# Performance work log

Hardware: AMD Instinct MI355X
Metric: run time of the kernel (lower is better)

The kernel has to match this reference:

```python
import jax, jax.numpy as jnp
import numpy as np
import math

B, LQ, LK = 4, 1024, 2048
QD, KD, VD = 768, 512, 512
H, NH = 1024, 16
HD = H // NH

def setup_inputs() -> dict:
    key = jax.random.key(0)
    ks = jax.random.split(key, 11)
    s = 0.02
    return {
        "query": jax.random.normal(ks[0], (B, LQ, QD), jnp.float32),
        "key": jax.random.normal(ks[1], (B, LK, KD), jnp.float32),
        "value": jax.random.normal(ks[2], (B, LK, VD), jnp.float32),
        "Wq": jax.random.normal(ks[3], (QD, H), jnp.float32) * s,
        "bq": jnp.zeros((H,), jnp.float32),
        "Wk": jax.random.normal(ks[4], (KD, H), jnp.float32) * s,
        "bk": jnp.zeros((H,), jnp.float32),
        "Wv": jax.random.normal(ks[5], (VD, H), jnp.float32) * s,
        "bv": jnp.zeros((H,), jnp.float32),
        "Wo": jax.random.normal(ks[6], (H, H), jnp.float32) * s,
        "bo": jnp.zeros((H,), jnp.float32),
    }

def reference(query, key, value, Wq, bq, Wk, bk, Wv, bv, Wo, bo):
    # project and split heads: [B, L, H] -> [B, NH, L, HD]
    def heads(x):
        b, l, _ = x.shape
        return x.reshape(b, l, NH, HD).transpose(0, 2, 1, 3)
    q = heads(query @ Wq + bq)   # [B, NH, LQ, HD]
    k = heads(key @ Wk + bk)     # [B, NH, LK, HD]
    v = heads(value @ Wv + bv)   # [B, NH, LK, HD]
    scores = jnp.einsum('bhqd,bhkd->bhqk', q, k) / math.sqrt(HD)
    weights = jax.nn.softmax(scores, axis=-1)  # dropout inactive (eval / rate used deterministically as identity)
    att = jnp.einsum('bhqk,bhkd->bhqd', weights, v)
    att = att.transpose(0, 2, 1, 3).reshape(query.shape[0], -1, H)
    out = att @ Wo + bo
    return out
```

## Files before the change

### kernel.cpp

```cpp
#include <hip/hip_runtime.h>
#include <math.h>

using bf16x8 = __attribute__((ext_vector_type(8))) short;
using f32x4  = __attribute__((ext_vector_type(4))) float;
using f32x16 = __attribute__((ext_vector_type(16))) float;

namespace {
constexpr int kB  = 4;
constexpr int kLQ = 1024;
constexpr int kLK = 2048;
constexpr int kH  = 1024;
constexpr int kHD = 64;
}

__device__ __forceinline__ unsigned short f2bf(float x) {
  union { float f; unsigned int u; } v; v.f = x;
  unsigned int r = v.u + 0x7fffu + ((v.u >> 16) & 1u);
  return (unsigned short)(r >> 16);
}
__device__ __forceinline__ unsigned int bfT(float x) {
  union { float f; unsigned int u; } v; v.f = x;
  return v.u >> 16;
}

typedef const __attribute__((address_space(1))) unsigned int guint_t;
typedef __attribute__((address_space(3))) unsigned int luint_t;
__device__ __forceinline__ void g2l16(const void* g, void* l) {
  __builtin_amdgcn_global_load_lds(
      (guint_t*)g,
      (luint_t*)(unsigned int)(unsigned long long)l,
      16, 0, 0);
}

__global__ __launch_bounds__(256) void prep_kernel(
    const float* __restrict__ q, const float* __restrict__ k,
    const float* __restrict__ v, const float* __restrict__ Wq,
    const float* __restrict__ Wk, const float* __restrict__ Wv,
    const float* __restrict__ Wo, unsigned short* __restrict__ qo,
    unsigned short* __restrict__ ko, unsigned short* __restrict__ vo,
    unsigned short* __restrict__ WqT, unsigned short* __restrict__ WkT,
    unsigned short* __restrict__ WvT, unsigned short* __restrict__ WoT)
{
  __shared__ float tile[64][65];
  const int t = threadIdx.x;
  if (blockIdx.x < 5632) {
    int c = blockIdx.x * 256 + t;
    const float* src; unsigned short* dst;
    if (c < 393216)      { src = q; dst = qo; }
    else if (c < 917504) { src = k; dst = ko; c -= 393216; }
    else                 { src = v; dst = vo; c -= 917504; }
    const int i = c * 8;
    const float4 a = *(const float4*)(src + i);
    const float4 b = *(const float4*)(src + i + 4);
    uint4 o;
    o.x = (unsigned int)f2bf(a.x) | ((unsigned int)f2bf(a.y) << 16);
    o.y = (unsigned int)f2bf(a.z) | ((unsigned int)f2bf(a.w) << 16);
    o.z = (unsigned int)f2bf(b.x) | ((unsigned int)f2bf(b.y) << 16);
    o.w = (unsigned int)f2bf(b.z) | ((unsigned int)f2bf(b.w) << 16);
    *(uint4*)(dst + i) = o;
    return;
  }
  int id = blockIdx.x - 5632;
  const float* W; unsigned short* Wt; int Kd;
  if (id < 192)      { W = Wq; Wt = WqT; Kd = 768; }
  else if (id < 320) { W = Wk; Wt = WkT; Kd = 512;  id -= 192; }
  else if (id < 448) { W = Wv; Wt = WvT; Kd = 512;  id -= 320; }
  else               { W = Wo; Wt = WoT; Kd = 1024; id -= 448; }
  const int Nd = 1024;
  const int n0 = (id & 15) * 64;
  const int k0 = (id >> 4) * 64;
  const int rr = t >> 4;
  const int c4 = t & 15;
#pragma unroll
  for (int i = 0; i < 4; ++i) {
    const int row = i * 16 + rr;
    const float4 vv = *(const float4*)(W + (size_t)(k0 + row) * Nd + n0 + c4 * 4);
    tile[row][c4*4+0] = vv.x; tile[row][c4*4+1] = vv.y;
    tile[row][c4*4+2] = vv.z; tile[row][c4*4+3] = vv.w;
  }
  __syncthreads();
#pragma unroll
  for (int i = 0; i < 4; ++i) {
    const int n = i * 16 + rr;
    ushort4 o;
    o.x = f2bf(tile[c4*4+0][n]); o.y = f2bf(tile[c4*4+1][n]);
    o.z = f2bf(tile[c4*4+2][n]); o.w = f2bf(tile[c4*4+3][n]);
    *(ushort4*)(Wt + (size_t)(n0 + n) * Kd + k0 + c4 * 4) = o;
  }
}

__device__ __forceinline__ void gemm_body256(
    const unsigned short* __restrict__ A, const unsigned short* __restrict__ Bt,
    const float* __restrict__ bias, unsigned short* __restrict__ Cout,
    int N, int K, int bx, int by, int mode, char* lds)
{
  const int t    = threadIdx.x;
  const int lane = t & 63;
  const int w    = t >> 6;
  const int l15  = lane & 15;
  const int lq8  = (lane >> 4) * 8;
  const int lq4  = (lane >> 4) * 4;
  const int r0   = by * 128;
  const int c0   = bx * 256;
  const int wm   = w >> 1, wn = w & 1;

  f32x4 acc[4][8] = {};

#pragma unroll
  for (int i = 0; i < 6; ++i) {
    const int g = w * 6 + i;
    const unsigned short* src = (g < 8) ? A : Bt;
    const int rbase = (g < 8) ? (r0 + g * 16) : (c0 + (g - 8) * 16);
    g2l16(src + (size_t)(rbase + l15) * K + lq8, lds + g * 1024 + lane * 16);
  }

  int pb = 0;
  for (int k0 = 0; k0 < K; k0 += 32, pb ^= 1) {
    __syncthreads();
    char* buf = lds + pb * 24576;
    if (k0 + 32 < K) {
      char* nbuf = lds + (pb ^ 1) * 24576;
#pragma unroll
      for (int i = 0; i < 6; ++i) {
        const int g = w * 6 + i;
        const unsigned short* src = (g < 8) ? A : Bt;
        const int rbase = (g < 8) ? (r0 + g * 16) : (c0 + (g - 8) * 16);
        g2l16(src + (size_t)(rbase + l15) * K + k0 + 32 + lq8, nbuf + g * 1024 + lane * 16);
      }
    }
    bf16x8 af[4], bfr[8];
#pragma unroll
    for (int i = 0; i < 4; ++i) af[i]  = *(const bf16x8*)(buf + (wm*4 + i) * 1024 + lane * 16);
#pragma unroll
    for (int j = 0; j < 8; ++j) bfr[j] = *(const bf16x8*)(buf + 8192 + (wn*8 + j) * 1024 + lane * 16);
#pragma unroll
    for (int i = 0; i < 4; ++i)
#pragma unroll
      for (int j = 0; j < 8; ++j)
        acc[i][j] = __builtin_amdgcn_mfma_f32_16x16x32_bf16(af[i], bfr[j], acc[i][j], 0, 0, 0);
  }

#pragma unroll
  for (int j = 0; j < 8; ++j) {
    const int col = c0 + wn * 128 + j * 16 + l15;
    const float bcol = bias[col];
#pragma unroll
    for (int i = 0; i < 4; ++i) {
      const int row = r0 + wm * 64 + i * 16 + lq4;
      if (mode == 1) {
#pragma unroll
        for (int r = 0; r < 4; ++r) Cout[(size_t)(row + r) * N + col] = f2bf(acc[i][j][r] + bcol);
      } else {
        const int bb = row >> 11;
        const int lk = row & 2047;
        ushort4 o;
        o.x = f2bf(acc[i][j][0] + bcol); o.y = f2bf(acc[i][j][1] + bcol);
        o.z = f2bf(acc[i][j][2] + bcol); o.w = f2bf(acc[i][j][3] + bcol);
        *(ushort4*)(Cout + (size_t)(bb * kH + col) * kLK + lk) = o;
      }
    }
  }
}

__global__ __launch_bounds__(256) void qkv_gemm_kernel(
    const unsigned short* __restrict__ qA, const unsigned short* __restrict__ WqT,
    const float* __restrict__ bq, unsigned short* __restrict__ Qb,
    const unsigned short* __restrict__ kA, const unsigned short* __restrict__ WkT,
    const float* __restrict__ bk, unsigned short* __restrict__ Kb,
    const unsigned short* __restrict__ vA, const unsigned short* __restrict__ WvT,
    const float* __restrict__ bv, unsigned short* __restrict__ Vtw)
{
  __shared__ __align__(16) char lds[49152];
  int id = blockIdx.x;
  if (id < 128) {
    gemm_body256(qA, WqT, bq, Qb, 1024, 768, id & 3, id >> 2, 1, lds);
  } else if (id < 384) {
    id -= 128;
    gemm_body256(kA, WkT, bk, Kb, 1024, 512, id & 3, id >> 2, 1, lds);
  } else {
    id -= 384;
    gemm_body256(vA, WvT, bv, Vtw, 1024, 512, id & 3, id >> 2, 2, lds);
  }
}

__global__ __launch_bounds__(256) void out_gemm_kernel(
    const unsigned short* __restrict__ A, const unsigned short* __restrict__ Bt,
    const float* __restrict__ bias, float* __restrict__ C)
{
  __shared__ __align__(16) char lds[32768];
  const int t    = threadIdx.x;
  const int lane = t & 63;
  const int w    = t >> 6;
  const int l15  = lane & 15;
  const int lq8  = (lane >> 4) * 8;
  const int lq4  = (lane >> 4) * 4;
  const int r0   = blockIdx.y * 128;
  const int c0   = blockIdx.x * 128;
  const int wm   = w >> 1, wn = w & 1;
  const int N = 1024, K = 1024;

  f32x4 acc[4][4] = {};

#pragma unroll
  for (int i = 0; i < 4; ++i) {
    const int g = w * 4 + i;
    const unsigned short* src = (g < 8) ? A : Bt;
    const int rbase = (g < 8) ? (r0 + g * 16) : (c0 + (g - 8) * 16);
    g2l16(src + (size_t)(rbase + l15) * K + lq8, lds + g * 1024 + lane * 16);
  }
  int pb = 0;
  for (int k0 = 0; k0 < K; k0 += 32, pb ^= 1) {
    __syncthreads();
    char* buf = lds + pb * 16384;
    if (k0 + 32 < K) {
      char* nbuf = lds + (pb ^ 1) * 16384;
#pragma unroll
      for (int i = 0; i < 4; ++i) {
        const int g = w * 4 + i;
        const unsigned short* src = (g < 8) ? A : Bt;
        const int rbase = (g < 8) ? (r0 + g * 16) : (c0 + (g - 8) * 16);
        g2l16(src + (size_t)(rbase + l15) * K + k0 + 32 + lq8, nbuf + g * 1024 + lane * 16);
      }
    }
    bf16x8 af[4], bfr[4];
#pragma unroll
    for (int i = 0; i < 4; ++i) af[i]  = *(const bf16x8*)(buf + (wm*4 + i) * 1024 + lane * 16);
#pragma unroll
    for (int j = 0; j < 4; ++j) bfr[j] = *(const bf16x8*)(buf + 8192 + (wn*4 + j) * 1024 + lane * 16);
#pragma unroll
    for (int i = 0; i < 4; ++i)
#pragma unroll
      for (int j = 0; j < 4; ++j)
        acc[i][j] = __builtin_amdgcn_mfma_f32_16x16x32_bf16(af[i], bfr[j], acc[i][j], 0, 0, 0);
  }
#pragma unroll
  for (int j = 0; j < 4; ++j) {
    const int col = c0 + wn * 64 + j * 16 + l15;
    const float bcol = bias[col];
#pragma unroll
    for (int i = 0; i < 4; ++i) {
      const int row = r0 + wm * 64 + i * 16 + lq4;
#pragma unroll
      for (int r = 0; r < 4; ++r) C[(size_t)(row + r) * N + col] = acc[i][j][r] + bcol;
    }
  }
}

__global__ __launch_bounds__(256) void attn_mfma_kernel(
    const unsigned short* __restrict__ Q, const unsigned short* __restrict__ K,
    const unsigned short* __restrict__ Vt, float* __restrict__ Op0,
    float* __restrict__ Op1, float* __restrict__ Ls)
{
  __shared__ __align__(16) char lds[65536];
  const int t    = threadIdx.x;
  const int lane = t & 63;
  const int w    = t >> 6;
  const int l31  = lane & 31;
  const int h    = lane >> 5;
  const int flat = blockIdx.x;
  const int bh   = flat & 63;
  const int g8   = flat >> 6;
  const int s    = g8 & 1;
  const int qb   = g8 >> 1;
  const int hh   = bh & 15;
  const int b    = bh >> 4;
  const int q0   = qb * 256;
  const int kcb  = s * 1024;
  const int hoff = hh * kHD;
  const int qw   = q0 + w * 64;

  bf16x8 qf[2][4];
#pragma unroll
  for (int qt2 = 0; qt2 < 2; ++qt2)
#pragma unroll
    for (int ds_ = 0; ds_ < 4; ++ds_)
      qf[qt2][ds_] = *(const bf16x8*)(Q + (size_t)(b*kLQ + qw + qt2*32 + l31) * kH
                                        + hoff + ds_*16 + h*8);

  f32x16 oacc[2][2] = {};
  float lsum[2] = {0.f, 0.f};

#pragma unroll
  for (int i = 0; i < 4; ++i) {
    const int g = w * 4 + i;
    if (g < 8) {
      g2l16(K + (size_t)(b*kLK + kcb + (g >> 2)*32 + l31) * kH + hoff + (g & 3)*16 + h*8,
            lds + g * 1024 + lane * 16);
    } else {
      const int gg = g - 8;
      g2l16(Vt + (size_t)(b*kH + hoff + (gg >> 2)*32 + l31) * kLK + kcb + (gg & 3)*16 + h*8,
            lds + 16384 + gg * 1024 + lane * 16);
    }
  }

  char* const pbase = lds + 32768 + w * 8192;

  for (int kt = 0; kt < 16; ++kt) {
    __syncthreads();
    char* kbuf = lds + (kt & 1) * 8192;
    char* vbuf = lds + 16384 + (kt & 1) * 8192;
    if (kt + 1 < 16) {
      char* nk = lds + ((kt + 1) & 1) * 8192;
      char* nv = lds + 16384 + ((kt + 1) & 1) * 8192;
      const int kc1 = kcb + (kt + 1) * 64;
#pragma unroll
      for (int i = 0; i < 4; ++i) {
        const int g = w * 4 + i;
        if (g < 8) {
          g2l16(K + (size_t)(b*kLK + kc1 + (g >> 2)*32 + l31) * kH + hoff + (g & 3)*16 + h*8,
                nk + g * 1024 + lane * 16);
        } else {
          const int gg = g - 8;
          g2l16(Vt + (size_t)(b*kH + hoff + (gg >> 2)*32 + l31) * kLK + kc1 + (gg & 3)*16 + h*8,
                nv + gg * 1024 + lane * 16);
        }
      }
    }

    f32x16 sacc[2][2] = {};
#pragma unroll
    for (int ds_ = 0; ds_ < 4; ++ds_) {
      const bf16x8 kf0 = *(const bf16x8*)(kbuf + (0*4 + ds_) * 1024 + lane * 16);
      const bf16x8 kf1 = *(const bf16x8*)(kbuf + (1*4 + ds_) * 1024 + lane * 16);
#pragma unroll
      for (int qt2 = 0; qt2 < 2; ++qt2) {
        sacc[0][qt2] = __builtin_amdgcn_mfma_f32_32x32x16_bf16(kf0, qf[qt2][ds_], sacc[0][qt2], 0, 0, 0);
        sacc[1][qt2] = __builtin_amdgcn_mfma_f32_32x32x16_bf16(kf1, qf[qt2][ds_], sacc[1][qt2], 0, 0, 0);
      }
    }

#pragma unroll
    for (int kct2 = 0; kct2 < 2; ++kct2)
#pragma unroll
      for (int qt2 = 0; qt2 < 2; ++qt2)
#pragma unroll
        for (int g4 = 0; g4 < 4; ++g4) {
          const float e0 = __builtin_amdgcn_exp2f(sacc[kct2][qt2][g4*4+0] * 0.18033688011112042f);
          const float e1 = __builtin_amdgcn_exp2f(sacc[kct2][qt2][g4*4+1] * 0.18033688011112042f);
          const float e2 = __builtin_amdgcn_exp2f(sacc[kct2][qt2][g4*4+2] * 0.18033688011112042f);
          const float e3 = __builtin_amdgcn_exp2f(sacc[kct2][qt2][g4*4+3] * 0.18033688011112042f);
          lsum[qt2] += (e0 + e1) + (e2 + e3);
          uint2 u;
          u.x = bfT(e0) | (bfT(e1) << 16);
          u.y = bfT(e2) | (bfT(e3) << 16);
          *(uint2*)(pbase + (qt2*4 + kct2*2 + (g4 >> 1)) * 1024 +
                    (((g4 & 1) * 32) + l31) * 16 + 8*h) = u;
        }

#pragma unroll
    for (int ks = 0; ks < 4; ++ks) {
      const bf16x8 pf0 = *(const bf16x8*)(pbase + (0*4 + ks) * 1024 + lane * 16);
      const bf16x8 pf1 = *(const bf16x8*)(pbase + (1*4 + ks) * 1024 + lane * 16);
      const bf16x8 vf0 = *(const bf16x8*)(vbuf + (0*4 + ks) * 1024 + lane * 16);
      const bf16x8 vf1 = *(const bf16x8*)(vbuf + (1*4 + ks) * 1024 + lane * 16);
      oacc[0][0] = __builtin_amdgcn_mfma_f32_32x32x16_bf16(pf0, vf0, oacc[0][0], 0, 0, 0);
      oacc[0][1] = __builtin_amdgcn_mfma_f32_32x32x16_bf16(pf0, vf1, oacc[0][1], 0, 0, 0);
      oacc[1][0] = __builtin_amdgcn_mfma_f32_32x32x16_bf16(pf1, vf0, oacc[1][0], 0, 0, 0);
      oacc[1][1] = __builtin_amdgcn_mfma_f32_32x32x16_bf16(pf1, vf1, oacc[1][1], 0, 0, 0);
    }
  }

#pragma unroll
  for (int qt2 = 0; qt2 < 2; ++qt2)
    lsum[qt2] += __shfl_xor(lsum[qt2], 32);

  float* Op = s ? Op1 : Op0;
#pragma unroll
  for (int qt2 = 0; qt2 < 2; ++qt2)
#pragma unroll
    for (int dt = 0; dt < 2; ++dt)
#pragma unroll
      for (int r = 0; r < 16; ++r) {
        const int qrow = qw + qt2*32 + (r & 3) + 8*(r >> 2) + 4*h;
        Op[(size_t)bh * 65536 + (size_t)qrow * 64 + dt*32 + l31] = oacc[qt2][dt][r];
      }
  if (h == 0) {
#pragma unroll
    for (int qt2 = 0; qt2 < 2; ++qt2)
      Ls[(size_t)s * 65536 + bh * 1024 + qw + qt2*32 + l31] = lsum[qt2];
  }
}

__global__ __launch_bounds__(256) void attn_reduce_kernel(
    const float* __restrict__ Op0, const float* __restrict__ Op1,
    const float* __restrict__ Ls, unsigned short* __restrict__ Ab)
{
  const int g   = blockIdx.x * 256 + threadIdx.x;
  const int bhq = g >> 3;
  const int d8  = (g & 7) * 8;
  const float inv = 1.f / (Ls[bhq] + Ls[65536 + bhq]);
  const size_t base = (size_t)bhq * 64 + d8;
  const float4 a0 = *(const float4*)(Op0 + base);
  const float4 a1 = *(const float4*)(Op0 + base + 4);
  const float4 b0 = *(const float4*)(Op1 + base);
  const float4 b1 = *(const float4*)(Op1 + base + 4);
  const int bh = bhq >> 10, qq = bhq & 1023;
  const int bb = bh >> 4, hh = bh & 15;
  unsigned short* dst = Ab + (size_t)(bb * kLQ + qq) * kH + hh * 64 + d8;
  ushort4 o0, o1;
  o0.x = f2bf((a0.x + b0.x) * inv); o0.y = f2bf((a0.y + b0.y) * inv);
  o0.z = f2bf((a0.z + b0.z) * inv); o0.w = f2bf((a0.w + b0.w) * inv);
  o1.x = f2bf((a1.x + b1.x) * inv); o1.y = f2bf((a1.y + b1.y) * inv);
  o1.z = f2bf((a1.z + b1.z) * inv); o1.w = f2bf((a1.w + b1.w) * inv);
  *(ushort4*)dst = o0;
  *(ushort4*)(dst + 4) = o1;
}

extern "C" void kernel_launch(void* const* d_in, const int* in_sizes, int n_in,
                              void* d_out, int out_size, void* d_ws, size_t ws_size,
                              hipStream_t stream) {
  (void)in_sizes; (void)n_in; (void)out_size; (void)ws_size;
  const float* query = (const float*)d_in[0];
  const float* key   = (const float*)d_in[1];
  const float* value = (const float*)d_in[2];
  const float* Wq = (const float*)d_in[3];
  const float* bq = (const float*)d_in[4];
  const float* Wk = (const float*)d_in[5];
  const float* bk = (const float*)d_in[6];
  const float* Wv = (const float*)d_in[7];
  const float* bv = (const float*)d_in[8];
  const float* Wo = (const float*)d_in[9];
  const float* bo = (const float*)d_in[10];
  float* out = (float*)d_out;

  unsigned short* ws  = (unsigned short*)d_ws;
  unsigned short* qA  = ws;
  unsigned short* kA  = qA  + 3145728;
  unsigned short* vA  = kA  + 4194304;
  unsigned short* WqT = vA  + 4194304;
  unsigned short* WkT = WqT + 786432;
  unsigned short* WvT = WkT + 524288;
  unsigned short* WoT = WvT + 524288;
  unsigned short* Qb  = WoT + 1048576;
  unsigned short* Kb  = Qb  + 4194304;
  unsigned short* Vtw = Kb  + 8388608;
  unsigned short* Ab  = Vtw + 8388608;

  float* Op0 = (float*)ws;
  float* Lsp = Op0 + 4194304;
  float* Op1 = (float*)(Ab + 4194304);

  dim3 blk(256);
  prep_kernel<<<6336, blk, 0, stream>>>(query, key, value, Wq, Wk, Wv, Wo,
                                        qA, kA, vA, WqT, WkT, WvT, WoT);
  qkv_gemm_kernel<<<640, blk, 0, stream>>>(qA, WqT, bq, Qb,
                                           kA, WkT, bk, Kb,
                                           vA, WvT, bv, Vtw);
  attn_mfma_kernel<<<512, blk, 0, stream>>>(Qb, Kb, Vtw, Op0, Op1, Lsp);
  attn_reduce_kernel<<<2048, blk, 0, stream>>>(Op0, Op1, Lsp, Ab);
  out_gemm_kernel<<<dim3(8, 32), blk, 0, stream>>>(Ab, WoT, bo, out);
}
```

Before: 265.4 us.

## Drop split-K attention and reduce kernel; use smaller 2-wave blocks with fused normalization

The attention kernel no longer splits the key range into two halves written as fp32 partials and later combined by a separate reduce kernel. Each block now has 2 waves, handles 64 queries over the full 2048 keys, and normalizes by the row sum before writing bf16 output directly. This removes the partial-output round trip through memory and one kernel launch, and LDS use per block drops to 40KB. In exchange, each wave covers half as many queries per K/V tile, so K/V reuse is lower and each block runs a sequential key loop twice as long.

```diff
diff --git a/kernel.cpp b/kernel.cpp
--- a/kernel.cpp
+++ b/kernel.cpp
@@ -246,12 +246,11 @@
   }
 }
 
-__global__ __launch_bounds__(256) void attn_mfma_kernel(
+__global__ __launch_bounds__(128) void attn_mfma_kernel(
     const unsigned short* __restrict__ Q, const unsigned short* __restrict__ K,
-    const unsigned short* __restrict__ Vt, float* __restrict__ Op0,
-    float* __restrict__ Op1, float* __restrict__ Ls)
-{
-  __shared__ __align__(16) char lds[65536];
+    const unsigned short* __restrict__ Vt, unsigned short* __restrict__ O)
+{
+  __shared__ __align__(16) char lds[40960];
   const int t    = threadIdx.x;
   const int lane = t & 63;
   const int w    = t >> 6;
@@ -259,53 +258,46 @@
   const int h    = lane >> 5;
   const int flat = blockIdx.x;
   const int bh   = flat & 63;
-  const int g8   = flat >> 6;
-  const int s    = g8 & 1;
-  const int qb   = g8 >> 1;
+  const int qb   = flat >> 6;
   const int hh   = bh & 15;
   const int b    = bh >> 4;
-  const int q0   = qb * 256;
-  const int kcb  = s * 1024;
+  const int q0   = qb * 64;
   const int hoff = hh * kHD;
-  const int qw   = q0 + w * 64;
-
-  bf16x8 qf[2][4];
-#pragma unroll
-  for (int qt2 = 0; qt2 < 2; ++qt2)
-#pragma unroll
-    for (int ds_ = 0; ds_ < 4; ++ds_)
-      qf[qt2][ds_] = *(const bf16x8*)(Q + (size_t)(b*kLQ + qw + qt2*32 + l31) * kH
-                                        + hoff + ds_*16 + h*8);
-
-  f32x16 oacc[2][2] = {};
-  float lsum[2] = {0.f, 0.f};
-
-#pragma unroll
-  for (int i = 0; i < 4; ++i) {
-    const int g = w * 4 + i;
+  const int qw   = q0 + w * 32;
+
+  bf16x8 qf[4];
+#pragma unroll
+  for (int ds_ = 0; ds_ < 4; ++ds_)
+    qf[ds_] = *(const bf16x8*)(Q + (size_t)(b*kLQ + qw + l31) * kH + hoff + ds_*16 + h*8);
+
+  f32x16 oacc[2] = {};
+  float lsum = 0.f;
+  char* const pw = lds + 32768 + w * 4096;
+
+#pragma unroll
+  for (int i = 0; i < 8; ++i) {
+    const int g = w * 8 + i;
     if (g < 8) {
-      g2l16(K + (size_t)(b*kLK + kcb + (g >> 2)*32 + l31) * kH + hoff + (g & 3)*16 + h*8,
+      g2l16(K + (size_t)(b*kLK + (g >> 2)*32 + l31) * kH + hoff + (g & 3)*16 + h*8,
             lds + g * 1024 + lane * 16);
     } else {
       const int gg = g - 8;
-      g2l16(Vt + (size_t)(b*kH + hoff + (gg >> 2)*32 + l31) * kLK + kcb + (gg & 3)*16 + h*8,
+      g2l16(Vt + (size_t)(b*kH + hoff + (gg >> 2)*32 + l31) * kLK + (gg & 3)*16 + h*8,
             lds + 16384 + gg * 1024 + lane * 16);
     }
   }
 
-  char* const pbase = lds + 32768 + w * 8192;
-
-  for (int kt = 0; kt < 16; ++kt) {
+  for (int kt = 0; kt < 32; ++kt) {
     __syncthreads();
     char* kbuf = lds + (kt & 1) * 8192;
     char* vbuf = lds + 16384 + (kt & 1) * 8192;
-    if (kt + 1 < 16) {
+    if (kt + 1 < 32) {
+      const int kc1 = (kt + 1) * 64;
       char* nk = lds + ((kt + 1) & 1) * 8192;
       char* nv = lds + 16384 + ((kt + 1) & 1) * 8192;
-      const int kc1 = kcb + (kt + 1) * 64;
-#pragma unroll
-      for (int i = 0; i < 4; ++i) {
-        const int g = w * 4 + i;
+#pragma unroll
+      for (int i = 0; i < 8; ++i) {
+        const int g = w * 8 + i;
         if (g < 8) {
           g2l16(K + (size_t)(b*kLK + kc1 + (g >> 2)*32 + l31) * kH + hoff + (g & 3)*16 + h*8,
                 nk + g * 1024 + lane * 16);
@@ -317,93 +309,53 @@
       }
     }
 
-    f32x16 sacc[2][2] = {};
+    f32x16 sacc[2] = {};
 #pragma unroll
     for (int ds_ = 0; ds_ < 4; ++ds_) {
       const bf16x8 kf0 = *(const bf16x8*)(kbuf + (0*4 + ds_) * 1024 + lane * 16);
       const bf16x8 kf1 = *(const bf16x8*)(kbuf + (1*4 + ds_) * 1024 + lane * 16);
-#pragma unroll
-      for (int qt2 = 0; qt2 < 2; ++qt2) {
-        sacc[0][qt2] = __builtin_amdgcn_mfma_f32_32x32x16_bf16(kf0, qf[qt2][ds_], sacc[0][qt2], 0, 0, 0);
-        sacc[1][qt2] = __builtin_amdgcn_mfma_f32_32x32x16_bf16(kf1, qf[qt2][ds_], sacc[1][qt2], 0, 0, 0);
-      }
-    }
-
-#pragma unroll
-    for (int kct2 = 0; kct2 < 2; ++kct2)
-#pragma unroll
-      for (int qt2 = 0; qt2 < 2; ++qt2)
-#pragma unroll
-        for (int g4 = 0; g4 < 4; ++g4) {
-          const float e0 = __builtin_amdgcn_exp2f(sacc[kct2][qt2][g4*4+0] * 0.18033688011112042f);
-          const float e1 = __builtin_amdgcn_exp2f(sacc[kct2][qt2][g4*4+1] * 0.18033688011112042f);
-          const float e2 = __builtin_amdgcn_exp2f(sacc[kct2][qt2][g4*4+2] * 0.18033688011112042f);
-          const float e3 = __builtin_amdgcn_exp2f(sacc[kct2][qt2][g4*4+3] * 0.18033688011112042f);
-          lsum[qt2] += (e0 + e1) + (e2 + e3);
-          uint2 u;
-          u.x = bfT(e0) | (bfT(e1) << 16);
-          u.y = bfT(e2) | (bfT(e3) << 16);
-          *(uint2*)(pbase + (qt2*4 + kct2*2 + (g4 >> 1)) * 1024 +
-                    (((g4 & 1) * 32) + l31) * 16 + 8*h) = u;
-        }
+      sacc[0] = __builtin_amdgcn_mfma_f32_32x32x16_bf16(kf0, qf[ds_], sacc[0], 0, 0, 0);
+      sacc[1] = __builtin_amdgcn_mfma_f32_32x32x16_bf16(kf1, qf[ds_], sacc[1], 0, 0, 0);
+    }
+
+#pragma unroll
+    for (int kct = 0; kct < 2; ++kct)
+#pragma unroll
+      for (int g4 = 0; g4 < 4; ++g4) {
+        const float e0 = __builtin_amdgcn_exp2f(sacc[kct][g4*4+0] * 0.18033688011112042f);
+        const float e1 = __builtin_amdgcn_exp2f(sacc[kct][g4*4+1] * 0.18033688011112042f);
+        const float e2 = __builtin_amdgcn_exp2f(sacc[kct][g4*4+2] * 0.18033688011112042f);
+        const float e3 = __builtin_amdgcn_exp2f(sacc[kct][g4*4+3] * 0.18033688011112042f);
+        lsum += (e0 + e1) + (e2 + e3);
+        uint2 u;
+        u.x = bfT(e0) | (bfT(e1) << 16);
+        u.y = bfT(e2) | (bfT(e3) << 16);
+        *(uint2*)(pw + kct*2048 + g4*512 + l31*16 + h*8) = u;
+      }
 
 #pragma unroll
     for (int ks = 0; ks < 4; ++ks) {
-      const bf16x8 pf0 = *(const bf16x8*)(pbase + (0*4 + ks) * 1024 + lane * 16);
-      const bf16x8 pf1 = *(const bf16x8*)(pbase + (1*4 + ks) * 1024 + lane * 16);
+      const bf16x8 pf  = *(const bf16x8*)(pw + ks * 1024 + lane * 16);
       const bf16x8 vf0 = *(const bf16x8*)(vbuf + (0*4 + ks) * 1024 + lane * 16);
       const bf16x8 vf1 = *(const bf16x8*)(vbuf + (1*4 + ks) * 1024 + lane * 16);
-      oacc[0][0] = __builtin_amdgcn_mfma_f32_32x32x16_bf16(pf0, vf0, oacc[0][0], 0, 0, 0);
-      oacc[0][1] = __builtin_amdgcn_mfma_f32_32x32x16_bf16(pf0, vf1, oacc[0][1], 0, 0, 0);
-      oacc[1][0] = __builtin_amdgcn_mfma_f32_32x32x16_bf16(pf1, vf0, oacc[1][0], 0, 0, 0);
-      oacc[1][1] = __builtin_amdgcn_mfma_f32_32x32x16_bf16(pf1, vf1, oacc[1][1], 0, 0, 0);
-    }
-  }
-
-#pragma unroll
-  for (int qt2 = 0; qt2 < 2; ++qt2)
-    lsum[qt2] += __shfl_xor(lsum[qt2], 32);
-
-  float* Op = s ? Op1 : Op0;
-#pragma unroll
-  for (int qt2 = 0; qt2 < 2; ++qt2)
-#pragma unroll
-    for (int dt = 0; dt < 2; ++dt)
-#pragma unroll
-      for (int r = 0; r < 16; ++r) {
-        const int qrow = qw + qt2*32 + (r & 3) + 8*(r >> 2) + 4*h;
-        Op[(size_t)bh * 65536 + (size_t)qrow * 64 + dt*32 + l31] = oacc[qt2][dt][r];
-      }
-  if (h == 0) {
-#pragma unroll
-    for (int qt2 = 0; qt2 < 2; ++qt2)
-      Ls[(size_t)s * 65536 + bh * 1024 + qw + qt2*32 + l31] = lsum[qt2];
-  }
-}
-
-__global__ __launch_bounds__(256) void attn_reduce_kernel(
-    const float* __restrict__ Op0, const float* __restrict__ Op1,
-    const float* __restrict__ Ls, unsigned short* __restrict__ Ab)
-{
-  const int g   = blockIdx.x * 256 + threadIdx.x;
-  const int bhq = g >> 3;
-  const int d8  = (g & 7) * 8;
-  const float inv = 1.f / (Ls[bhq] + Ls[65536 + bhq]);
-  const size_t base = (size_t)bhq * 64 + d8;
-  const float4 a0 = *(const float4*)(Op0 + base);
-  const float4 a1 = *(const float4*)(Op0 + base + 4);
-  const float4 b0 = *(const float4*)(Op1 + base);
-  const float4 b1 = *(const float4*)(Op1 + base + 4);
-  const int bh = bhq >> 10, qq = bhq & 1023;
-  const int bb = bh >> 4, hh = bh & 15;
-  unsigned short* dst = Ab + (size_t)(bb * kLQ + qq) * kH + hh * 64 + d8;
-  ushort4 o0, o1;
-  o0.x = f2bf((a0.x + b0.x) * inv); o0.y = f2bf((a0.y + b0.y) * inv);
-  o0.z = f2bf((a0.z + b0.z) * inv); o0.w = f2bf((a0.w + b0.w) * inv);
-  o1.x = f2bf((a1.x + b1.x) * inv); o1.y = f2bf((a1.y + b1.y) * inv);
-  o1.z = f2bf((a1.z + b1.z) * inv); o1.w = f2bf((a1.w + b1.w) * inv);
-  *(ushort4*)dst = o0;
-  *(ushort4*)(dst + 4) = o1;
+      oacc[0] = __builtin_amdgcn_mfma_f32_32x32x16_bf16(pf, vf0, oacc[0], 0, 0, 0);
+      oacc[1] = __builtin_amdgcn_mfma_f32_32x32x16_bf16(pf, vf1, oacc[1], 0, 0, 0);
+    }
+  }
+
+  lsum += __shfl_xor(lsum, 32);
+  __syncthreads();
+  if (h == 0) *(float*)(pw + l31 * 4) = 1.f / lsum;
+  __syncthreads();
+
+#pragma unroll
+  for (int dt = 0; dt < 2; ++dt)
+#pragma unroll
+    for (int r = 0; r < 16; ++r) {
+      const int ql = (r & 3) + 8 * (r >> 2) + 4 * h;
+      const float inv = *(const float*)(pw + ql * 4);
+      O[(size_t)(b*kLQ + qw + ql) * kH + hoff + dt*32 + l31] = f2bf(oacc[dt][r] * inv);
+    }
 }
 
 extern "C" void kernel_launch(void* const* d_in, const int* in_sizes, int n_in,
@@ -436,17 +388,12 @@
   unsigned short* Vtw = Kb  + 8388608;
   unsigned short* Ab  = Vtw + 8388608;
 
-  float* Op0 = (float*)ws;
-  float* Lsp = Op0 + 4194304;
-  float* Op1 = (float*)(Ab + 4194304);
-
   dim3 blk(256);
   prep_kernel<<<6336, blk, 0, stream>>>(query, key, value, Wq, Wk, Wv, Wo,
                                         qA, kA, vA, WqT, WkT, WvT, WoT);
   qkv_gemm_kernel<<<640, blk, 0, stream>>>(qA, WqT, bq, Qb,
                                            kA, WkT, bk, Kb,
                                            vA, WvT, bv, Vtw);
-  attn_mfma_kernel<<<512, blk, 0, stream>>>(Qb, Kb, Vtw, Op0, Op1, Lsp);
-  attn_reduce_kernel<<<2048, blk, 0, stream>>>(Op0, Op1, Lsp, Ab);
+  attn_mfma_kernel<<<1024, dim3(128), 0, stream>>>(Qb, Kb, Vtw, Ab);
   out_gemm_kernel<<<dim3(8, 32), blk, 0, stream>>>(Ab, WoT, bo, out);
 }
```

New measurement: 261.0 us. About the same (-1.7%).
